# Performance work log

Hardware: AMD Instinct MI355X
Metric: run time of the kernel (lower is better)

Reference implementation:

```python
import jax, jax.numpy as jnp
import numpy as np

N_NODES = 50000
N_EDGES = 800000
IN_C, HID_C, OUT_C = 256, 256, 128


def gcn_conv(x, W, b, row, col, n_nodes):
    """PyG GCNConv: linear transform, symmetric-normalized aggregation, bias.
    row/col already include self-loops. Messages flow row -> col."""
    h = x @ W  # [N, out]
    deg = jax.ops.segment_sum(jnp.ones_like(col, dtype=h.dtype), col, num_segments=n_nodes)
    d_inv_sqrt = jnp.where(deg > 0, jax.lax.rsqrt(jnp.maximum(deg, 1e-12)), 0.0)
    norm = d_inv_sqrt[row] * d_inv_sqrt[col]  # [E]
    msg = h[row] * norm[:, None]              # gather + scale, [E, out]
    out = jax.ops.segment_sum(msg, col, num_segments=n_nodes)  # scatter-add
    return out + b


def setup_inputs() -> dict:
    key = jax.random.key(0)
    k_x, k_e, k_w1, k_w2 = jax.random.split(key, 4)
    x = jax.random.normal(k_x, (N_NODES, IN_C), dtype=jnp.float32)
    edge_index = jax.random.randint(k_e, (2, N_EDGES), 0, N_NODES, dtype=jnp.int64)
    # Glorot-style init for GCN weights, zeros bias (PyG default)
    s1 = float(np.sqrt(6.0 / (IN_C + HID_C)))
    s2 = float(np.sqrt(6.0 / (HID_C + OUT_C)))
    W1 = jax.random.uniform(k_w1, (IN_C, HID_C), dtype=jnp.float32, minval=-s1, maxval=s1)
    b1 = jnp.zeros((HID_C,), dtype=jnp.float32)
    W2 = jax.random.uniform(k_w2, (HID_C, OUT_C), dtype=jnp.float32, minval=-s2, maxval=s2)
    b2 = jnp.zeros((OUT_C,), dtype=jnp.float32)
    return {"x": x, "edge_index": edge_index, "W1": W1, "b1": b1, "W2": W2, "b2": b2}


def reference(x, edge_index, W1, b1, W2, b2):
    n = x.shape[0]
    # add self-loops (PyG GCNConv default add_self_loops=True)
    loops = jnp.arange(n, dtype=edge_index.dtype)
    row = jnp.concatenate([edge_index[0], loops])
    col = jnp.concatenate([edge_index[1], loops])
    h = gcn_conv(x, W1, b1, row, col, n)
    h = jax.nn.relu(h)  # dropout p=0.0 -> identity
    out = gcn_conv(h, W2, b2, row, col, n)
    return out
```

## Files before the change

### kernel.cpp

```cpp
#include <hip/hip_runtime.h>

#define NN 50000
#define NE 800000
#define IN_C 256
#define HID_C 256
#define OUT_C 128

#define NBUCK 196
#define CHUNK 4096
#define NPA 196
#define CAP_B 5120

typedef unsigned short u16;
typedef __attribute__((ext_vector_type(8))) short short8;
typedef __attribute__((ext_vector_type(8))) unsigned short ushort8;
typedef __attribute__((ext_vector_type(4))) float f32x4;

__device__ __forceinline__ u16 f2b(float f) {
  unsigned int u = __float_as_uint(f);
  return (u16)((u + 0x7FFFu + ((u >> 16) & 1u)) >> 16);
}
__device__ __forceinline__ float b2f(u16 s) {
  return __uint_as_float(((unsigned int)s) << 16);
}


__global__ __launch_bounds__(256) void convw_zero(const float* __restrict__ W1,
                                                  const float* __restrict__ W2,
                                                  u16* __restrict__ W1t,
                                                  u16* __restrict__ W2t,
                                                  int* __restrict__ cnt,
                                                  u16* __restrict__ Hbz,
                                                  u16* __restrict__ H3z,
                                                  int nzb) {
  int b = blockIdx.x;
  if (b < 256) {
    int id = b * 256 + threadIdx.x;
    if (id < 256 * 256) {
      int n = id >> 8, k = id & 255;
      W1t[id] = f2b(W1[k * 256 + n]);
    }
    if (id < 128 * 256) {
      int n = id >> 8, k = id & 255;
      W2t[id] = f2b(W2[k * 128 + n]);
    }
  } else if (b < 256 + nzb) {
    int i = (b - 256) * 256 + threadIdx.x;
    if (i < NN) cnt[i] = 0;
  } else {
    if (threadIdx.x < 256) Hbz[threadIdx.x] = 0;
    if (threadIdx.x < 128) H3z[threadIdx.x] = 0;
  }
}


__global__ __launch_bounds__(256) void hist_kernel(const int* __restrict__ col,
                                                   int* __restrict__ cnt, int E) {
  int e = blockIdx.x * blockDim.x + threadIdx.x;
  if (e < E) atomicAdd(&cnt[col[e]], 1);
}

__global__ __launch_bounds__(256) void scan1_kernel(const int* __restrict__ cnt,
                                                    int* __restrict__ bsum, int n) {
  __shared__ int ws[4];
  int i = blockIdx.x * 256 + threadIdx.x;
  int lane = threadIdx.x & 63, wid = threadIdx.x >> 6;
  int v = (i < n) ? cnt[i] : 0;
#pragma unroll
  for (int off = 32; off > 0; off >>= 1) v += __shfl_down(v, off, 64);
  if (lane == 0) ws[wid] = v;
  __syncthreads();
  if (threadIdx.x == 0) bsum[blockIdx.x] = ws[0] + ws[1] + ws[2] + ws[3];
}

__global__ __launch_bounds__(256) void scan2_kernel(const int* __restrict__ bsum,
                                                    int* __restrict__ boff,
                                                    int* __restrict__ row_off,
                                                    int nb, int n) {
  __shared__ int wsum[4], wpre[5];
  int lane = threadIdx.x & 63, wid = threadIdx.x >> 6;
  int v = (threadIdx.x < nb) ? bsum[threadIdx.x] : 0;
  int s = v;
#pragma unroll
  for (int off = 1; off < 64; off <<= 1) {
    int t = __shfl_up(s, off, 64);
    if (lane >= off) s += t;
  }
  if (lane == 63) wsum[wid] = s;
  __syncthreads();
  if (threadIdx.x == 0) {
    int acc = 0;
#pragma unroll
    for (int w = 0; w < 4; ++w) { wpre[w] = acc; acc += wsum[w]; }
    wpre[4] = acc;
  }
  __syncthreads();
  if (threadIdx.x < nb) boff[threadIdx.x] = wpre[wid] + (s - v);
  if (threadIdx.x == 0) row_off[n] = wpre[4];
}

__global__ __launch_bounds__(256) void scan3_kernel(const int* __restrict__ cnt,
                                                    const int* __restrict__ boff,
                                                    int* __restrict__ row_off,
                                                    int* __restrict__ bcur,
                                                    float* __restrict__ dinv, int n) {
  __shared__ int wsum[4], wpre[4];
  int i = blockIdx.x * 256 + threadIdx.x;
  int lane = threadIdx.x & 63, wid = threadIdx.x >> 6;
  int v = (i < n) ? cnt[i] : 0;
  int s = v;
#pragma unroll
  for (int off = 1; off < 64; off <<= 1) {
    int t = __shfl_up(s, off, 64);
    if (lane >= off) s += t;
  }
  if (lane == 63) wsum[wid] = s;
  __syncthreads();
  if (threadIdx.x == 0) {
    int acc = 0;
#pragma unroll
    for (int w = 0; w < 4; ++w) { wpre[w] = acc; acc += wsum[w]; }
  }
  __syncthreads();
  if (i < n) {
    int off = boff[blockIdx.x] + wpre[wid] + (s - v);
    row_off[i] = off;
    if ((i & 255) == 0) bcur[i >> 8] = off;
    dinv[i] = rsqrtf((float)(v + 1));
  }
}


template <bool A_IS_F32>
__device__ __forceinline__ void gemm_body(const void* __restrict__ Ap,
                                          const u16* __restrict__ Bt,
                                          const float* __restrict__ dscale,
                                          u16* __restrict__ C, int M, int N,
                                          int bx, int by,
                                          u16 (&Asl)[2][5120], u16 (&Bsl)[2][5120]) {
  const int tid = threadIdx.x;
  const int row0 = by * 128;
  const int col0 = bx * 128;

  f32x4 acc[4][4] = {};

  const int seg = tid & 7;
  const int rb = tid >> 3;
  const int wave = tid >> 6, lane = tid & 63;
  const int wm = wave >> 1, wn = wave & 1;
  const int qr = lane & 15, quad = lane >> 4;

  float4 aF[4];
  ushort4 aU[4];
  ushort4 bR[4];

  auto load_tiles = [&](int k0) {
    if constexpr (A_IS_F32) {
      const float* A = (const float*)Ap;
#pragma unroll
      for (int i = 0; i < 4; ++i) {
        int gr = row0 + rb + i * 32;
        aF[i] = (gr < M) ? *(const float4*)&A[(size_t)gr * 256 + k0 + seg * 4]
                         : make_float4(0.f, 0.f, 0.f, 0.f);
      }
    } else {
      const u16* A = (const u16*)Ap;
#pragma unroll
      for (int i = 0; i < 4; ++i) {
        int gr = row0 + rb + i * 32;
        aU[i] = (gr < M) ? *(const ushort4*)&A[(size_t)gr * 256 + k0 + seg * 4]
                         : make_ushort4(0, 0, 0, 0);
      }
    }
#pragma unroll
    for (int i = 0; i < 4; ++i) {
      int n = rb + i * 32;
      bR[i] = *(const ushort4*)&Bt[(size_t)(col0 + n) * 256 + k0 + seg * 4];
    }
  };

  auto write_lds = [&](int buf) {
#pragma unroll
    for (int i = 0; i < 4; ++i) {
      int r = rb + i * 32;
      ushort4 u;
      if constexpr (A_IS_F32) {
        u.x = f2b(aF[i].x); u.y = f2b(aF[i].y);
        u.z = f2b(aF[i].z); u.w = f2b(aF[i].w);
      } else {
        u = aU[i];
      }
      *(ushort4*)&Asl[buf][r * 40 + seg * 4] = u;
      *(ushort4*)&Bsl[buf][r * 40 + seg * 4] = bR[i];
    }
  };

  load_tiles(0);
  write_lds(0);
  __syncthreads();

#pragma unroll
  for (int it = 0; it < 8; ++it) {
    const int cur = it & 1;
    if (it < 7) load_tiles((it + 1) * 32);

    short8 afr[4], bfr[4];
#pragma unroll
    for (int mt = 0; mt < 4; ++mt)
      afr[mt] = *(const short8*)&Asl[cur][(wm * 64 + mt * 16 + qr) * 40 + quad * 8];
#pragma unroll
    for (int nt = 0; nt < 4; ++nt)
      bfr[nt] = *(const short8*)&Bsl[cur][(wn * 64 + nt * 16 + qr) * 40 + quad * 8];
#pragma unroll
    for (int mt = 0; mt < 4; ++mt)
#pragma unroll
      for (int nt = 0; nt < 4; ++nt)
        acc[mt][nt] = __builtin_amdgcn_mfma_f32_16x16x32_bf16(afr[mt], bfr[nt], acc[mt][nt], 0, 0, 0);

    if (it < 7) {
      write_lds(1 - cur);
      __syncthreads();
    }
  }

#pragma unroll
  for (int mt = 0; mt < 4; ++mt) {
#pragma unroll
    for (int i = 0; i < 4; ++i) {
      int gr = row0 + wm * 64 + mt * 16 + quad * 4 + i;
      if (gr < M) {
        float sc = dscale[gr];
#pragma unroll
        for (int nt = 0; nt < 4; ++nt) {
          int gc = col0 + wn * 64 + nt * 16 + qr;
          C[(size_t)gr * N + gc] = f2b(acc[mt][nt][i] * sc);
        }
      }
    }
  }
}

template <bool A_IS_F32>
__global__ __launch_bounds__(256) void gemm_mfma(const void* __restrict__ Ap,
                                                 const u16* __restrict__ Bt,
                                                 const float* __restrict__ dscale,
                                                 u16* __restrict__ C, int M, int N) {
  __shared__ u16 Asl[2][5120];
  __shared__ u16 Bsl[2][5120];
  gemm_body<A_IS_F32>(Ap, Bt, dscale, C, M, N, blockIdx.x, blockIdx.y, Asl, Bsl);
}

__global__ __launch_bounds__(256) void gemm1_scatter(const float* __restrict__ x,
                                                     const u16* __restrict__ W1t,
                                                     const float* __restrict__ dinv,
                                                     u16* __restrict__ Hb, int M, int N,
                                                     int ngb,
                                                     const int* __restrict__ row,
                                                     const int* __restrict__ col,
                                                     int* __restrict__ bcur,
                                                     uint2* __restrict__ stage, int E) {
  __shared__ u16 ABsl[4][5120];
  int b = blockIdx.x;
  if (b < ngb) {
    gemm_body<true>(x, W1t, dinv, Hb, M, N, b & 1, b >> 1,
                    *reinterpret_cast<u16(*)[2][5120]>(&ABsl[0]),
                    *reinterpret_cast<u16(*)[2][5120]>(&ABsl[2]));
  } else {
    uint2* pairs = (uint2*)ABsl;
    int* hcnt = (int*)((char*)ABsl + 32768);
    int* hscan = hcnt + 256;
    int* hbase = hscan + 256;
    int* lcur = hbase + 256;

    const int tid = threadIdx.x;
    const int blk = b - ngb;
    const int e0 = blk * CHUNK;

    hcnt[tid] = 0;
    __syncthreads();

    int ecol[16], erow[16];
#pragma unroll
    for (int j = 0; j < 16; ++j) {
      int e = e0 + j * 256 + tid;
      if (e < E) {
        ecol[j] = col[e];
        erow[j] = row[e];
        atomicAdd(&hcnt[ecol[j] >> 8], 1);
      } else {
        ecol[j] = -1;
      }
    }
    __syncthreads();

    hscan[tid] = hcnt[tid];
    __syncthreads();
#pragma unroll
    for (int off = 1; off < 256; off <<= 1) {
      int t = (tid >= off) ? hscan[tid - off] : 0;
      __syncthreads();
      hscan[tid] += t;
      __syncthreads();
    }

    lcur[tid] = 0;
    if (hcnt[tid] > 0) hbase[tid] = atomicAdd(&bcur[tid], hcnt[tid]);
    __syncthreads();

#pragma unroll
    for (int j = 0; j < 16; ++j) {
      if (ecol[j] >= 0) {
        int bk = ecol[j] >> 8;
        int p = atomicAdd(&lcur[bk], 1);
        pairs[(hscan[bk] - hcnt[bk]) + p] = make_uint2((unsigned)erow[j], (unsigned)ecol[j]);
      }
    }
    __syncthreads();

    int mtot = hscan[255];
    for (int s = tid; s < mtot; s += 256) {
      uint2 pr = pairs[s];
      int bk = (int)(pr.y >> 8);
      stage[hbase[bk] + (s - (hscan[bk] - hcnt[bk]))] = pr;
    }
  }
}

__global__ __launch_bounds__(256) void csr_sort(const uint2* __restrict__ stage,
                                                const int* __restrict__ row_off,
                                                int* __restrict__ csr) {
  __shared__ int cur[256];
  __shared__ int outb[CAP_B];
  const int b = blockIdx.x;
  const int base_node = b << 8;
  const int nnodes = min(256, NN - base_node);
  const int tid = threadIdx.x;
  const int bstart = row_off[base_node];
  const int bend = row_off[min(base_node + 256, NN)];
  if (tid < nnodes) cur[tid] = row_off[base_node + tid] - bstart;
  __syncthreads();
  const int m = bend - bstart;
  for (int i = tid; i < m; i += 256) {
    uint2 pr = stage[bstart + i];
    int cl = min((int)pr.y - base_node, 255) & 255;
    int p = atomicAdd(&cur[cl], 1);
    if (p < CAP_B) outb[p] = (int)pr.x;
    else if (bstart + p < NE) csr[bstart + p] = (int)pr.x;
  }
  __syncthreads();
  const int mm = min(m, CAP_B);
  for (int i = tid; i < mm; i += 256) csr[bstart + i] = outb[i];
}


template <int ROW_CH, int NSL, bool RELU_BF16>
__global__ __launch_bounds__(256) void agg_sliced2(const u16* __restrict__ h,
                                                   const int* __restrict__ row_off,
                                                   const int* __restrict__ csr,
                                                   const float* __restrict__ dinv,
                                                   const float* __restrict__ bias,
                                                   void* __restrict__ outp, int n) {
  constexpr int SH = (ROW_CH == 256) ? 8 : 7;
  const int slice = blockIdx.x % NSL;
  const int wave = threadIdx.x >> 6;
  const int lane = threadIdx.x & 63;
  const int nd = lane >> 5;
  const int l5 = lane & 31;
  const int eg = l5 >> 3;
  const int c0 = slice * 64 + (l5 & 7) * 8;
  const int v = (blockIdx.x / NSL) * 8 + wave * 2 + nd;
  const int beg = row_off[v], end = row_off[v + 1];
  const int srcl = (nd << 5) + eg;

  float a[8] = {};
  for (int base = beg; base < end; base += 16) {
    int p = base + (l5 & 15);
    int idx = (p < end) ? csr[p] : NN;
    unsigned s0 = (unsigned)__shfl(idx, srcl, 64);
    unsigned s1 = (unsigned)__shfl(idx, srcl + 4, 64);
    unsigned s2 = (unsigned)__shfl(idx, srcl + 8, 64);
    unsigned s3 = (unsigned)__shfl(idx, srcl + 12, 64);
    ushort8 g0 = *(const ushort8*)&h[(s0 << SH) + c0];
    ushort8 g1 = *(const ushort8*)&h[(s1 << SH) + c0];
    ushort8 g2 = *(const ushort8*)&h[(s2 << SH) + c0];
    ushort8 g3 = *(const ushort8*)&h[(s3 << SH) + c0];
#pragma unroll
    for (int i = 0; i < 8; ++i) {
      a[i] += b2f((u16)g0[i]);
      a[i] += b2f((u16)g1[i]);
      a[i] += b2f((u16)g2[i]);
      a[i] += b2f((u16)g3[i]);
    }
  }
#pragma unroll
  for (int i = 0; i < 8; ++i) {
    a[i] += __shfl_xor(a[i], 8, 64);
    a[i] += __shfl_xor(a[i], 16, 64);
  }
  if (eg == 0) {
    ushort8 hs = *(const ushort8*)&h[((unsigned)v << SH) + c0];
    float dv = dinv[v];
    float4 bv0 = *(const float4*)&bias[c0];
    float4 bv1 = *(const float4*)&bias[c0 + 4];
    float bb[8] = {bv0.x, bv0.y, bv0.z, bv0.w, bv1.x, bv1.y, bv1.z, bv1.w};
    if constexpr (RELU_BF16) {
      u16* out = (u16*)outp;
      ushort8 o;
#pragma unroll
      for (int i = 0; i < 8; ++i) {
        float r = fmaxf((a[i] + b2f((u16)hs[i])) * dv + bb[i], 0.f);
        o[i] = (short)f2b(r);
      }
      *(ushort8*)&out[((size_t)v << SH) + c0] = o;
    } else {
      float* out = (float*)outp;
      float o[8];
#pragma unroll
      for (int i = 0; i < 8; ++i) o[i] = (a[i] + b2f((u16)hs[i])) * dv + bb[i];
      *(float4*)&out[((size_t)v << SH) + c0] = make_float4(o[0], o[1], o[2], o[3]);
      *(float4*)&out[((size_t)v << SH) + c0 + 4] = make_float4(o[4], o[5], o[6], o[7]);
    }
  }
}


extern "C" void kernel_launch(void* const* d_in, const int* in_sizes, int n_in,
                              void* d_out, int out_size, void* d_ws, size_t ws_size,
                              hipStream_t stream) {
  const float* x = (const float*)d_in[0];
  const int* ei = (const int*)d_in[1];
  const float* W1 = (const float*)d_in[2];
  const float* b1 = (const float*)d_in[3];
  const float* W2 = (const float*)d_in[4];
  const float* b2 = (const float*)d_in[5];
  float* out = (float*)d_out;

  const int* row = ei;
  const int* col = ei + NE;

  const int NB = (NN + 255) / 256;

  u16* Hb = (u16*)d_ws;
  u16* H2b = Hb + (size_t)(NN + 1) * 256;
  u16* H3b = H2b + (size_t)NN * 256;
  u16* W1t = H3b + (size_t)(NN + 1) * 128;
  u16* W2t = W1t + 256 * 256;
  int* cnt = (int*)(W2t + 128 * 256);
  int* row_off = cnt + NN;
  int* bcur = row_off + NN + 4;
  float* dinv = (float*)(bcur + 256);
  int* bsum = (int*)(dinv + NN);
  int* boff = bsum + 200;
  int* csr = boff + 200;
  uint2* stage = (uint2*)H3b;

  convw_zero<<<256 + NB + 1, 256, 0, stream>>>(W1, W2, W1t, W2t, cnt,
                                               Hb + (size_t)NN * 256,
                                               H3b + (size_t)NN * 128, NB);
  hist_kernel<<<(NE + 255) / 256, 256, 0, stream>>>(col, cnt, NE);
  scan1_kernel<<<NB, 256, 0, stream>>>(cnt, bsum, NN);
  scan2_kernel<<<1, 256, 0, stream>>>(bsum, boff, row_off, NB, NN);
  scan3_kernel<<<NB, 256, 0, stream>>>(cnt, boff, row_off, bcur, dinv, NN);

  {
    const int ngb = (HID_C / 128) * ((NN + 127) / 128);
    gemm1_scatter<<<ngb + NPA, 256, 0, stream>>>(x, W1t, dinv, Hb, NN, HID_C, ngb,
                                                 row, col, bcur, stage, NE);
  }
  csr_sort<<<NBUCK, 256, 0, stream>>>(stage, row_off, csr);

  agg_sliced2<256, 4, true><<<(NN / 8) * 4, 256, 0, stream>>>(
      Hb, row_off, csr, dinv, b1, H2b, NN);

  {
    dim3 grid(OUT_C / 128, (NN + 127) / 128);
    gemm_mfma<false><<<grid, 256, 0, stream>>>(H2b, W2t, dinv, H3b, NN, OUT_C);
  }

  agg_sliced2<128, 2, false><<<(NN / 8) * 2, 256, 0, stream>>>(
      H3b, row_off, csr, dinv, b2, out, NN);
}
```

Before: 269.6 us.

## Store GEMM outputs in 32-channel planar layout for sliced aggregation gathers

The GEMM epilogues now write H and H3 as planes of 32 channels per node, [plane][node][32], instead of row-major. The aggregation kernel is rewritten to gather 64-byte contiguous rows per plane, handling 4 nodes per wave with packed float2 accumulation. The intent is better cache-line locality for the random neighbor gathers, since each slice touches a compact plane, and cheaper bf16-to-f32 accumulation. The cost is scattered 2-byte stores in the GEMM epilogue and more blocks in the aggregation launch. The padding zero row is now written into each plane, for H1 by convw_zero and for H3 inside the second GEMM launch.

```diff
diff --git a/kernel.cpp b/kernel.cpp
--- a/kernel.cpp
+++ b/kernel.cpp
@@ -15,6 +15,9 @@
 typedef __attribute__((ext_vector_type(8))) short short8;
 typedef __attribute__((ext_vector_type(8))) unsigned short ushort8;
 typedef __attribute__((ext_vector_type(4))) float f32x4;
+typedef __attribute__((ext_vector_type(2))) float f32x2;
+
+#define CPS ((size_t)(NN + 1) * 32)
 
 __device__ __forceinline__ u16 f2b(float f) {
   unsigned int u = __float_as_uint(f);
@@ -30,8 +33,7 @@
                                                   u16* __restrict__ W1t,
                                                   u16* __restrict__ W2t,
                                                   int* __restrict__ cnt,
-                                                  u16* __restrict__ Hbz,
-                                                  u16* __restrict__ H3z,
+                                                  u16* __restrict__ Hb,
                                                   int nzb) {
   int b = blockIdx.x;
   if (b < 256) {
@@ -48,8 +50,8 @@
     int i = (b - 256) * 256 + threadIdx.x;
     if (i < NN) cnt[i] = 0;
   } else {
-    if (threadIdx.x < 256) Hbz[threadIdx.x] = 0;
-    if (threadIdx.x < 128) H3z[threadIdx.x] = 0;
+    int t = threadIdx.x;
+    Hb[(size_t)(t >> 5) * CPS + (size_t)NN * 32 + (t & 31)] = 0;
   }
 }
 
@@ -131,7 +133,7 @@
 }
 
 
-template <bool A_IS_F32>
+template <bool A_IS_F32, bool PLANAR_C>
 __device__ __forceinline__ void gemm_body(const void* __restrict__ Ap,
                                           const u16* __restrict__ Bt,
                                           const float* __restrict__ dscale,
@@ -233,21 +235,30 @@
 #pragma unroll
         for (int nt = 0; nt < 4; ++nt) {
           int gc = col0 + wn * 64 + nt * 16 + qr;
-          C[(size_t)gr * N + gc] = f2b(acc[mt][nt][i] * sc);
+          u16 val = f2b(acc[mt][nt][i] * sc);
+          if constexpr (PLANAR_C)
+            C[(size_t)(gc >> 5) * CPS + (size_t)gr * 32 + (gc & 31)] = val;
+          else
+            C[(size_t)gr * N + gc] = val;
         }
       }
     }
   }
 }
 
-template <bool A_IS_F32>
+template <bool A_IS_F32, bool PLANAR_C>
 __global__ __launch_bounds__(256) void gemm_mfma(const void* __restrict__ Ap,
                                                  const u16* __restrict__ Bt,
                                                  const float* __restrict__ dscale,
-                                                 u16* __restrict__ C, int M, int N) {
+                                                 u16* __restrict__ C, int M, int N,
+                                                 u16* __restrict__ zrow) {
+  if (zrow != nullptr && blockIdx.x == 0 && blockIdx.y == 0 && threadIdx.x < 128) {
+    int t = threadIdx.x;
+    zrow[(size_t)(t >> 5) * CPS + (size_t)NN * 32 + (t & 31)] = 0;
+  }
   __shared__ u16 Asl[2][5120];
   __shared__ u16 Bsl[2][5120];
-  gemm_body<A_IS_F32>(Ap, Bt, dscale, C, M, N, blockIdx.x, blockIdx.y, Asl, Bsl);
+  gemm_body<A_IS_F32, PLANAR_C>(Ap, Bt, dscale, C, M, N, blockIdx.x, blockIdx.y, Asl, Bsl);
 }
 
 __global__ __launch_bounds__(256) void gemm1_scatter(const float* __restrict__ x,
@@ -262,9 +273,9 @@
   __shared__ u16 ABsl[4][5120];
   int b = blockIdx.x;
   if (b < ngb) {
-    gemm_body<true>(x, W1t, dinv, Hb, M, N, b & 1, b >> 1,
-                    *reinterpret_cast<u16(*)[2][5120]>(&ABsl[0]),
-                    *reinterpret_cast<u16(*)[2][5120]>(&ABsl[2]));
+    gemm_body<true, true>(x, W1t, dinv, Hb, M, N, b & 1, b >> 1,
+                          *reinterpret_cast<u16(*)[2][5120]>(&ABsl[0]),
+                          *reinterpret_cast<u16(*)[2][5120]>(&ABsl[2]));
   } else {
     uint2* pairs = (uint2*)ABsl;
     int* hcnt = (int*)((char*)ABsl + 32768);
@@ -353,55 +364,58 @@
 }
 
 
-template <int ROW_CH, int NSL, bool RELU_BF16>
-__global__ __launch_bounds__(256) void agg_sliced2(const u16* __restrict__ h,
-                                                   const int* __restrict__ row_off,
-                                                   const int* __restrict__ csr,
-                                                   const float* __restrict__ dinv,
-                                                   const float* __restrict__ bias,
-                                                   void* __restrict__ outp, int n) {
-  constexpr int SH = (ROW_CH == 256) ? 8 : 7;
-  const int slice = blockIdx.x % NSL;
+template <int NPL, int OUTC, bool RELU_BF16>
+__global__ __launch_bounds__(256) void agg_planar(const u16* __restrict__ h,
+                                                  const int* __restrict__ row_off,
+                                                  const int* __restrict__ csr,
+                                                  const float* __restrict__ dinv,
+                                                  const float* __restrict__ bias,
+                                                  void* __restrict__ outp) {
+  const int slice = blockIdx.x % NPL;
   const int wave = threadIdx.x >> 6;
   const int lane = threadIdx.x & 63;
-  const int nd = lane >> 5;
-  const int l5 = lane & 31;
-  const int eg = l5 >> 3;
-  const int c0 = slice * 64 + (l5 & 7) * 8;
-  const int v = (blockIdx.x / NSL) * 8 + wave * 2 + nd;
+  const int nd = lane >> 4;
+  const int l4 = lane & 15;
+  const int eg = l4 >> 2;
+  const int co = l4 & 3;
+  const int coff = co * 8;
+  const int v = (blockIdx.x / NPL) * 16 + wave * 4 + nd;
+  const u16* hpl = h + (size_t)slice * CPS;
   const int beg = row_off[v], end = row_off[v + 1];
-  const int srcl = (nd << 5) + eg;
-
-  float a[8] = {};
+  const int sb = (lane & 48) + eg;
+
+  f32x2 accp[4] = {};
   for (int base = beg; base < end; base += 16) {
-    int p = base + (l5 & 15);
+    int p = base + l4;
     int idx = (p < end) ? csr[p] : NN;
-    unsigned s0 = (unsigned)__shfl(idx, srcl, 64);
-    unsigned s1 = (unsigned)__shfl(idx, srcl + 4, 64);
-    unsigned s2 = (unsigned)__shfl(idx, srcl + 8, 64);
-    unsigned s3 = (unsigned)__shfl(idx, srcl + 12, 64);
-    ushort8 g0 = *(const ushort8*)&h[(s0 << SH) + c0];
-    ushort8 g1 = *(const ushort8*)&h[(s1 << SH) + c0];
-    ushort8 g2 = *(const ushort8*)&h[(s2 << SH) + c0];
-    ushort8 g3 = *(const ushort8*)&h[(s3 << SH) + c0];
-#pragma unroll
-    for (int i = 0; i < 8; ++i) {
-      a[i] += b2f((u16)g0[i]);
-      a[i] += b2f((u16)g1[i]);
-      a[i] += b2f((u16)g2[i]);
-      a[i] += b2f((u16)g3[i]);
-    }
-  }
+#pragma unroll
+    for (int j = 0; j < 4; ++j) {
+      unsigned s = (unsigned)__shfl(idx, sb + j * 4, 64);
+      ushort8 g = *(const ushort8*)&hpl[(size_t)s * 32 + coff];
+      const unsigned* w = (const unsigned*)&g;
+#pragma unroll
+      for (int q = 0; q < 4; ++q) {
+        f32x2 val;
+        val[0] = __uint_as_float(w[q] << 16);
+        val[1] = __uint_as_float(w[q] & 0xffff0000u);
+        accp[q] += val;
+      }
+    }
+  }
+  float a[8];
+#pragma unroll
+  for (int q = 0; q < 4; ++q) { a[2 * q] = accp[q][0]; a[2 * q + 1] = accp[q][1]; }
 #pragma unroll
   for (int i = 0; i < 8; ++i) {
+    a[i] += __shfl_xor(a[i], 4, 64);
     a[i] += __shfl_xor(a[i], 8, 64);
-    a[i] += __shfl_xor(a[i], 16, 64);
   }
   if (eg == 0) {
-    ushort8 hs = *(const ushort8*)&h[((unsigned)v << SH) + c0];
+    const int cg = slice * 32 + coff;
+    ushort8 hs = *(const ushort8*)&hpl[(size_t)v * 32 + coff];
     float dv = dinv[v];
-    float4 bv0 = *(const float4*)&bias[c0];
-    float4 bv1 = *(const float4*)&bias[c0 + 4];
+    float4 bv0 = *(const float4*)&bias[cg];
+    float4 bv1 = *(const float4*)&bias[cg + 4];
     float bb[8] = {bv0.x, bv0.y, bv0.z, bv0.w, bv1.x, bv1.y, bv1.z, bv1.w};
     if constexpr (RELU_BF16) {
       u16* out = (u16*)outp;
@@ -411,14 +425,14 @@
         float r = fmaxf((a[i] + b2f((u16)hs[i])) * dv + bb[i], 0.f);
         o[i] = (short)f2b(r);
       }
-      *(ushort8*)&out[((size_t)v << SH) + c0] = o;
+      *(ushort8*)&out[(size_t)v * OUTC + cg] = o;
     } else {
       float* out = (float*)outp;
       float o[8];
 #pragma unroll
       for (int i = 0; i < 8; ++i) o[i] = (a[i] + b2f((u16)hs[i])) * dv + bb[i];
-      *(float4*)&out[((size_t)v << SH) + c0] = make_float4(o[0], o[1], o[2], o[3]);
-      *(float4*)&out[((size_t)v << SH) + c0 + 4] = make_float4(o[4], o[5], o[6], o[7]);
+      *(float4*)&out[(size_t)v * OUTC + cg] = make_float4(o[0], o[1], o[2], o[3]);
+      *(float4*)&out[(size_t)v * OUTC + cg + 4] = make_float4(o[4], o[5], o[6], o[7]);
     }
   }
 }
@@ -454,9 +468,7 @@
   int* csr = boff + 200;
   uint2* stage = (uint2*)H3b;
 
-  convw_zero<<<256 + NB + 1, 256, 0, stream>>>(W1, W2, W1t, W2t, cnt,
-                                               Hb + (size_t)NN * 256,
-                                               H3b + (size_t)NN * 128, NB);
+  convw_zero<<<256 + NB + 1, 256, 0, stream>>>(W1, W2, W1t, W2t, cnt, Hb, NB);
   hist_kernel<<<(NE + 255) / 256, 256, 0, stream>>>(col, cnt, NE);
   scan1_kernel<<<NB, 256, 0, stream>>>(cnt, bsum, NN);
   scan2_kernel<<<1, 256, 0, stream>>>(bsum, boff, row_off, NB, NN);
@@ -469,14 +481,14 @@
   }
   csr_sort<<<NBUCK, 256, 0, stream>>>(stage, row_off, csr);
 
-  agg_sliced2<256, 4, true><<<(NN / 8) * 4, 256, 0, stream>>>(
-      Hb, row_off, csr, dinv, b1, H2b, NN);
+  agg_planar<8, 256, true><<<(NN / 16) * 8, 256, 0, stream>>>(
+      Hb, row_off, csr, dinv, b1, H2b);
 
   {
     dim3 grid(OUT_C / 128, (NN + 127) / 128);
-    gemm_mfma<false><<<grid, 256, 0, stream>>>(H2b, W2t, dinv, H3b, NN, OUT_C);
-  }
-
-  agg_sliced2<128, 2, false><<<(NN / 8) * 2, 256, 0, stream>>>(
-      H3b, row_off, csr, dinv, b2, out, NN);
-}
+    gemm_mfma<false, true><<<grid, 256, 0, stream>>>(H2b, W2t, dinv, H3b, NN, OUT_C, H3b);
+  }
+
+  agg_planar<4, 128, false><<<(NN / 16) * 4, 256, 0, stream>>>(
+      H3b, row_off, csr, dinv, b2, out);
+}
```

After: 272.8 us. No clear change (+1.2%).
